# Performance work log

Hardware: AMD Instinct MI355X
Metric: run time of the kernel (lower is better)

The kernel has to match this reference:

```python
import jax, jax.numpy as jnp
import numpy as np
from jax import lax

B, S, D, E, H = 2, 2048, 1024, 8, 4096


def setup_inputs() -> dict:
    key = jax.random.key(0)
    ks = jax.random.split(key, 10)
    sc = 0.02  # GPT-style init scale
    return {
        "x": jax.random.normal(ks[0], (B, S, D), jnp.float32),
        "noise": jax.random.normal(ks[1], (B, S, E), jnp.float32),
        "w_route": jax.random.normal(ks[2], (D, E), jnp.float32) * sc,
        "b_route": jnp.zeros((E,), jnp.float32),
        "w_noise": jax.random.normal(ks[3], (D, E), jnp.float32) * sc,
        "b_noise": jnp.zeros((E,), jnp.float32),
        "w_fc": jax.random.normal(ks[4], (E, D, H), jnp.float32) * sc,
        "b_fc": jnp.zeros((E, H), jnp.float32),
        "w_proj": jax.random.normal(ks[5], (E, H, D), jnp.float32) * sc,
        "b_proj": jnp.zeros((E, D), jnp.float32),
        "top_k": 2,
    }


def reference(x, noise, w_route, b_route, w_noise, b_noise, w_fc, b_fc, w_proj, b_proj, top_k):
    # --- NoisyTopkRouter ---
    logits = x @ w_route + b_route                      # [B,S,E]
    noise_logits = x @ w_noise + b_noise                # [B,S,E]
    noisy = logits + noise * jax.nn.softplus(noise_logits)
    gate1 = jax.nn.softmax(noisy, axis=-1)              # dense gate (aux output)

    topk_vals, topk_idx = lax.top_k(noisy, top_k)       # [B,S,K]
    # softmax over sparse logits (-inf elsewhere) == softmax over the top-k values
    gk = jax.nn.softmax(topk_vals, axis=-1)             # [B,S,K]
    # scatter top-k gates back to the dense expert axis; non-selected experts get 0
    gating = (jax.nn.one_hot(topk_idx, E, dtype=x.dtype) * gk[..., None]).sum(-2)  # [B,S,E]

    # --- Experts (dense-over-experts, masked by gating; math identical to
    #     masked gather/scatter since non-selected gates are exactly 0) ---
    h = jnp.einsum('bsd,edh->bseh', x, w_fc) + b_fc     # [B,S,E,H]
    h = jax.nn.gelu(h, approximate=True)                # GELU(tanh)
    y = jnp.einsum('bseh,ehd->bsed', h, w_proj) + b_proj  # [B,S,E,D]
    out = jnp.einsum('bsed,bse->bsd', y, gating)        # weighted combine
    return out, gate1
```

## Files before the change

### kernel.cpp

```cpp
#include <hip/hip_runtime.h>
#include <cstdint>


#define DEV __device__ __forceinline__

typedef __attribute__((ext_vector_type(8))) short short8;
typedef __attribute__((ext_vector_type(4))) float floatx4;

constexpr int D_ = 1024, E_ = 8, H_ = 4096;
constexpr int NTOK = 4096;
constexpr int CAP  = 4096;
constexpr int TOTSLOT = NTOK * 2;

constexpr size_t O_COUNT = 0;
constexpr size_t O_OFFS  = 64;
constexpr size_t O_BTOK  = 128;
constexpr size_t O_BGATE = O_BTOK  + (size_t)E_ * CAP * 4;
constexpr size_t O_PAIR  = O_BGATE + (size_t)E_ * CAP * 4;
constexpr size_t O_XG    = (O_PAIR + (size_t)NTOK * 2 * 4 + 255) & ~(size_t)255;
constexpr size_t O_HBUF  = O_XG   + (size_t)TOTSLOT * D_ * 2;
constexpr size_t O_YBUF  = O_HBUF + (size_t)TOTSLOT * H_ * 2;
constexpr size_t O_WT    = O_YBUF + (size_t)TOTSLOT * D_ * 2;
constexpr size_t WS_NEED = O_WT   + (size_t)E_ * D_ * H_ * 2;

DEV float b2f(unsigned short u) {
    union { unsigned int i; float f; } v; v.i = ((unsigned int)u) << 16; return v.f;
}
DEV unsigned int f2b(float f) {
    union { float f; unsigned int i; } v; v.f = f;
    unsigned int r = v.i + 0x7fffu + ((v.i >> 16) & 1u);
    return (r >> 16) & 0xffffu;
}
DEV float gelu_tanh(float x) {
    float u = 0.7978845608028654f * (x + 0.044715f * x * x * x);
    u = fminf(fmaxf(u, -20.f), 20.f);
    float e = __expf(2.f * u);
    float t = (e - 1.f) / (e + 1.f);
    return 0.5f * x * (1.f + t);
}

typedef __attribute__((address_space(3))) unsigned int lds_u32_t;
typedef const __attribute__((address_space(1))) unsigned int g_u32_t;
DEV void gload16(const unsigned short* g, const unsigned short* l) {
    __builtin_amdgcn_global_load_lds((g_u32_t*)(size_t)g,
                                     (lds_u32_t*)(unsigned int)(size_t)l, 16, 0, 0);
}

__global__ __launch_bounds__(64) void zero_counts(int* counts) {
    if (threadIdx.x < E_) counts[threadIdx.x] = 0;
}

__global__ __launch_bounds__(256) void router_kernel(
    const float* __restrict__ x, const float* __restrict__ noise,
    const float* __restrict__ w_route, const float* __restrict__ b_route,
    const float* __restrict__ w_noise, const float* __restrict__ b_noise,
    float* __restrict__ out,
    int* counts, int* btok, float* bgate, int* pairs)
{
    int wave = threadIdx.x >> 6, lane = threadIdx.x & 63;
    int t = blockIdx.x * 4 + wave;

    double racc[E_], nacc[E_];
#pragma unroll
    for (int e = 0; e < E_; e++) { racc[e] = 0.0; nacc[e] = 0.0; }

#pragma unroll 4
    for (int i = 0; i < D_ / 64; i++) {
        int j = i * 64 + lane;
        float xv = x[(size_t)t * D_ + j];
        const float* wr = w_route + (size_t)j * E_;
        const float* wn = w_noise + (size_t)j * E_;
        float4 a0 = ((const float4*)wr)[0], a1 = ((const float4*)wr)[1];
        float4 c0 = ((const float4*)wn)[0], c1 = ((const float4*)wn)[1];
        const float rv[8] = {a0.x,a0.y,a0.z,a0.w,a1.x,a1.y,a1.z,a1.w};
        const float nv[8] = {c0.x,c0.y,c0.z,c0.w,c1.x,c1.y,c1.z,c1.w};
#pragma unroll
        for (int e = 0; e < E_; e++) {
            racc[e] += (double)(xv * rv[e]);
            nacc[e] += (double)(xv * nv[e]);
        }
    }
#pragma unroll
    for (int off = 32; off > 0; off >>= 1)
#pragma unroll
        for (int e = 0; e < E_; e++) {
            racc[e] += __shfl_down(racc[e], off);
            nacc[e] += __shfl_down(nacc[e], off);
        }

    if (lane == 0) {
        double nz[E_];
#pragma unroll
        for (int e = 0; e < E_; e++) {
            double lg = racc[e] + (double)b_route[e];
            double nl = nacc[e] + (double)b_noise[e];
            double sp = (nl > 0.0) ? nl + log1p(exp(-nl)) : log1p(exp(nl));
            nz[e] = lg + (double)noise[(size_t)t * E_ + e] * sp;
        }
        double mx = nz[0];
#pragma unroll
        for (int e = 1; e < E_; e++) mx = fmax(mx, nz[e]);
        double se = 0.0, ex[E_];
#pragma unroll
        for (int e = 0; e < E_; e++) { ex[e] = exp(nz[e] - mx); se += ex[e]; }
#pragma unroll
        for (int e = 0; e < E_; e++)
            out[(size_t)NTOK * D_ + (size_t)t * E_ + e] = (float)(ex[e] / se);
        double v0 = -1e300, v1 = -1e300; int i0 = 0, i1 = 0;
#pragma unroll
        for (int e = 0; e < E_; e++) {
            double v = nz[e];
            if (v > v0) { v1 = v0; i1 = i0; v0 = v; i0 = e; }
            else if (v > v1) { v1 = v; i1 = e; }
        }
        double g0 = 1.0 / (1.0 + exp(v1 - v0));
        float  g1 = (float)(1.0 - g0);
        int l0 = atomicAdd(&counts[i0], 1);
        int l1 = atomicAdd(&counts[i1], 1);
        btok[i0 * CAP + l0] = t;  bgate[i0 * CAP + l0] = (float)g0;
        btok[i1 * CAP + l1] = t;  bgate[i1 * CAP + l1] = g1;
        pairs[2 * t]     = (i0 << 16) | l0;
        pairs[2 * t + 1] = (i1 << 16) | l1;
    }
}

__global__ __launch_bounds__(64) void offsets_kernel(const int* counts, int* offs) {
    if (threadIdx.x == 0) {
        int a = 0;
        for (int e = 0; e < E_; e++) { offs[e] = a; a += counts[e]; }
        offs[E_] = a;
    }
}

__global__ __launch_bounds__(256) void gather_x(
    const float* __restrict__ x, const int* __restrict__ pairs,
    const int* __restrict__ offs, unsigned short* __restrict__ xg)
{
    int t = blockIdx.x;
    int c = threadIdx.x * 4;
    float4 v = *(const float4*)(x + (size_t)t * D_ + c);
    uint2 o;
    o.x = f2b(v.x) | (f2b(v.y) << 16);
    o.y = f2b(v.z) | (f2b(v.w) << 16);
    int p0 = pairs[2 * t], p1 = pairs[2 * t + 1];
    size_t r0 = (size_t)(offs[p0 >> 16] + (p0 & 0xffff)) * D_;
    size_t r1 = (size_t)(offs[p1 >> 16] + (p1 & 0xffff)) * D_;
    *(uint2*)(xg + r0 + c) = o;
    *(uint2*)(xg + r1 + c) = o;
}

__global__ __launch_bounds__(256) void transpose_w(
    const float* __restrict__ w, unsigned short* __restrict__ wT, int K, int N)
{
    __shared__ unsigned short t[64][65];
    const int e  = blockIdx.z;
    const int k0 = blockIdx.y * 64;
    const int n0 = blockIdx.x * 64;
    const int r  = threadIdx.x >> 2;
    const int c4 = (threadIdx.x & 3) * 16;
    const float* src = w + ((size_t)e * K + k0 + r) * N + n0 + c4;
#pragma unroll
    for (int i = 0; i < 4; i++) {
        float4 v = ((const float4*)src)[i];
        t[r][c4 + 4*i + 0] = (unsigned short)f2b(v.x);
        t[r][c4 + 4*i + 1] = (unsigned short)f2b(v.y);
        t[r][c4 + 4*i + 2] = (unsigned short)f2b(v.z);
        t[r][c4 + 4*i + 3] = (unsigned short)f2b(v.w);
    }
    __syncthreads();
    unsigned short* dstp = wT + ((size_t)e * N + n0 + r) * K + k0 + c4;
    unsigned short tmp[16];
#pragma unroll
    for (int i = 0; i < 16; i++) tmp[i] = t[c4 + i][r];
#pragma unroll
    for (int h = 0; h < 2; h++) {
        uint4 pk;
        pk.x = (unsigned int)tmp[8*h+0] | ((unsigned int)tmp[8*h+1] << 16);
        pk.y = (unsigned int)tmp[8*h+2] | ((unsigned int)tmp[8*h+3] << 16);
        pk.z = (unsigned int)tmp[8*h+4] | ((unsigned int)tmp[8*h+5] << 16);
        pk.w = (unsigned int)tmp[8*h+6] | ((unsigned int)tmp[8*h+7] << 16);
        ((uint4*)dstp)[h] = pk;
    }
}

template <int KD, int ND, bool FC>
__global__ __launch_bounds__(256) void moe_gemm3(
    const unsigned short* __restrict__ A,
    const unsigned short* __restrict__ wT,
    const float* __restrict__ bias32,
    unsigned short* __restrict__ dst,
    const int* __restrict__ counts, const int* __restrict__ offs,
    const float* __restrict__ bgate)
{
    const int lin = blockIdx.x;
    const int xcd = lin & 7, slot = lin >> 3;
    int e, mt, nt;
    if (FC) {
        nt = xcd * 4 + (slot & 3);
        mt = (slot >> 2) & 31;
        e  = slot >> 7;
    } else {
        nt = xcd;
        mt = slot & 31;
        e  = slot >> 5;
    }
    const int cnt = counts[e];
    const int m0 = mt * 128;
    if (m0 >= cnt) return;
    const int n0 = nt * 128;
    const int off = offs[e];

    __shared__ unsigned short smem[2][2 * 128 * 64];
    constexpr int BOFF = 128 * 64;

    const int tid = threadIdx.x;
    const int waveid = tid >> 6, lane = tid & 63;
    const int sr = lane >> 3;
    const int g  = lane & 7;
    const int scol = ((g ^ sr) * 8);

    const unsigned short* aAddr[4];
    const unsigned short* bAddr[4];
#pragma unroll
    for (int c = 0; c < 4; c++) {
        int ar = m0 + (waveid * 4 + c) * 8 + sr;
        if (ar > cnt - 1) ar = cnt - 1;
        aAddr[c] = A + (size_t)(off + ar) * KD + scol;
        int br = n0 + (waveid * 4 + c) * 8 + sr;
        bAddr[c] = wT + ((size_t)e * ND + br) * KD + scol;
    }
    const int ldsChunk = (waveid * 4) * 512;

    const int wm = (waveid & 1) * 64, wn = (waveid >> 1) * 64;
    const int lrow = lane & 15, quad = lane >> 4;

    floatx4 acc[4][4];
#pragma unroll
    for (int fm = 0; fm < 4; fm++)
#pragma unroll
        for (int fn = 0; fn < 4; fn++) acc[fm][fn] = (floatx4)0.f;

    const int nk = KD / 64;

#pragma unroll
    for (int c = 0; c < 4; c++) {
        gload16(aAddr[c], &smem[0][ldsChunk + c * 512]);
        gload16(bAddr[c], &smem[0][BOFF + ldsChunk + c * 512]);
    }
    __syncthreads();

#pragma unroll 2
    for (int t = 0; t < nk; ++t) {
        const int cur = t & 1;
        if (t + 1 < nk) {
            const int k0 = (t + 1) * 64;
#pragma unroll
            for (int c = 0; c < 4; c++) {
                gload16(aAddr[c] + k0, &smem[cur ^ 1][ldsChunk + c * 512]);
                gload16(bAddr[c] + k0, &smem[cur ^ 1][BOFF + ldsChunk + c * 512]);
            }
        }
        const unsigned short* As = &smem[cur][0];
        const unsigned short* Bs = &smem[cur][BOFF];
#pragma unroll
        for (int ks = 0; ks < 2; ks++) {
            short8 af[4], bfr[4];
#pragma unroll
            for (int f = 0; f < 4; f++) {
                int Ra = wm + f * 16 + lrow;
                int Rb = wn + f * 16 + lrow;
                af[f]  = *(const short8*)&As[Ra * 64 + ((ks * 4 + quad) ^ (Ra & 7)) * 8];
                bfr[f] = *(const short8*)&Bs[Rb * 64 + ((ks * 4 + quad) ^ (Rb & 7)) * 8];
            }
#pragma unroll
            for (int fm = 0; fm < 4; fm++)
#pragma unroll
                for (int fn = 0; fn < 4; fn++)
                    acc[fm][fn] = __builtin_amdgcn_mfma_f32_16x16x32_bf16(
                        af[fm], bfr[fn], acc[fm][fn], 0, 0, 0);
        }
        __syncthreads();
    }

    const int gc = n0 + wn + lrow;
    float bcol[4];
#pragma unroll
    for (int fn = 0; fn < 4; fn++) bcol[fn] = bias32[(size_t)e * ND + gc + fn * 16];

#pragma unroll
    for (int fm = 0; fm < 4; fm++) {
        int srow0 = m0 + wm + fm * 16 + quad * 4;
#pragma unroll
        for (int r = 0; r < 4; r++) {
            int srow = srow0 + r;
            if (srow < cnt) {
                size_t base = (size_t)(off + srow) * ND;
                if (FC) {
#pragma unroll
                    for (int fn = 0; fn < 4; fn++) {
                        float v = acc[fm][fn][r] + bcol[fn];
                        dst[base + gc + fn * 16] = (unsigned short)f2b(gelu_tanh(v));
                    }
                } else {
                    float gt = bgate[e * CAP + srow];
#pragma unroll
                    for (int fn = 0; fn < 4; fn++) {
                        float v = (acc[fm][fn][r] + bcol[fn]) * gt;
                        dst[base + gc + fn * 16] = (unsigned short)f2b(v);
                    }
                }
            }
        }
    }
}

__global__ __launch_bounds__(256) void combine_kernel(
    const unsigned short* __restrict__ ybuf, const int* __restrict__ pairs,
    const int* __restrict__ offs, float* __restrict__ out)
{
    int t = blockIdx.x;
    int p0 = pairs[2 * t], p1 = pairs[2 * t + 1];
    size_t r0 = (size_t)(offs[p0 >> 16] + (p0 & 0xffff)) * D_;
    size_t r1 = (size_t)(offs[p1 >> 16] + (p1 & 0xffff)) * D_;
    int c = threadIdx.x * 4;
    uint2 a = *(const uint2*)(ybuf + r0 + c);
    uint2 b = *(const uint2*)(ybuf + r1 + c);
    float4 o;
    o.x = b2f((unsigned short)(a.x & 0xffffu)) + b2f((unsigned short)(b.x & 0xffffu));
    o.y = b2f((unsigned short)(a.x >> 16))     + b2f((unsigned short)(b.x >> 16));
    o.z = b2f((unsigned short)(a.y & 0xffffu)) + b2f((unsigned short)(b.y & 0xffffu));
    o.w = b2f((unsigned short)(a.y >> 16))     + b2f((unsigned short)(b.y >> 16));
    *(float4*)(out + (size_t)t * D_ + c) = o;
}

extern "C" void kernel_launch(void* const* d_in, const int* in_sizes, int n_in,
                              void* d_out, int out_size, void* d_ws, size_t ws_size,
                              hipStream_t stream) {
    if (ws_size < WS_NEED) return;

    const float* x       = (const float*)d_in[0];
    const float* noise   = (const float*)d_in[1];
    const float* w_route = (const float*)d_in[2];
    const float* b_route = (const float*)d_in[3];
    const float* w_noise = (const float*)d_in[4];
    const float* b_noise = (const float*)d_in[5];
    const float* w_fc    = (const float*)d_in[6];
    const float* b_fc    = (const float*)d_in[7];
    const float* w_proj  = (const float*)d_in[8];
    const float* b_proj  = (const float*)d_in[9];

    char* ws = (char*)d_ws;
    int*   counts = (int*)(ws + O_COUNT);
    int*   offs   = (int*)(ws + O_OFFS);
    int*   btok   = (int*)(ws + O_BTOK);
    float* bgate  = (float*)(ws + O_BGATE);
    int*   pairs  = (int*)(ws + O_PAIR);
    unsigned short* xg   = (unsigned short*)(ws + O_XG);
    unsigned short* hbuf = (unsigned short*)(ws + O_HBUF);
    unsigned short* ybuf = (unsigned short*)(ws + O_YBUF);
    unsigned short* wT   = (unsigned short*)(ws + O_WT);

    zero_counts<<<dim3(1), dim3(64), 0, stream>>>(counts);
    router_kernel<<<dim3(NTOK / 4), dim3(256), 0, stream>>>(
        x, noise, w_route, b_route, w_noise, b_noise, (float*)d_out,
        counts, btok, bgate, pairs);
    offsets_kernel<<<dim3(1), dim3(64), 0, stream>>>(counts, offs);
    gather_x<<<dim3(NTOK), dim3(256), 0, stream>>>(x, pairs, offs, xg);

    transpose_w<<<dim3(H_ / 64, D_ / 64, E_), dim3(256), 0, stream>>>(w_fc, wT, D_, H_);
    moe_gemm3<D_, H_, true><<<dim3(8 * 32 * 32), dim3(256), 0, stream>>>(
        xg, wT, b_fc, hbuf, counts, offs, bgate);

    transpose_w<<<dim3(D_ / 64, H_ / 64, E_), dim3(256), 0, stream>>>(w_proj, wT, H_, D_);
    moe_gemm3<H_, D_, false><<<dim3(8 * 32 * 8), dim3(256), 0, stream>>>(
        hbuf, wT, b_proj, ybuf, counts, offs, bgate);

    combine_kernel<<<dim3(NTOK), dim3(256), 0, stream>>>(ybuf, pairs, offs, (float*)d_out);
}
```

Before: 685.1 us.

## Enlarge MoE GEMM tiles to 256-row blocks with 512 threads

Replaces the 128x128, 256-thread expert GEMM with a templated kernel that uses 256x256 tiles for the FC GEMM and 256x128 tiles for the projection GEMM. It runs 8 waves per block and moves the double buffer into dynamic LDS. The wave-to-tile mapping and the per-wave accumulator count are generalised, and the grid decomposition is recomputed for the larger tiles. The aim is more operand reuse per LDS load and fewer weight re-reads across M tiles. The costs are higher register pressure (up to 128 accumulator registers per lane), a very large LDS footprint (128KB for FC) that limits occupancy to one block per CU, and coarser padding waste on partially filled expert tiles.

```diff
diff --git a/kernel.cpp b/kernel.cpp
--- a/kernel.cpp
+++ b/kernel.cpp
@@ -183,8 +183,8 @@
     }
 }
 
-template <int KD, int ND, bool FC>
-__global__ __launch_bounds__(256) void moe_gemm3(
+template <int BM, int BN, int KD, int ND, bool FC>
+__global__ __launch_bounds__(512, 2) void moe_gemm_big(
     const unsigned short* __restrict__ A,
     const unsigned short* __restrict__ wT,
     const float* __restrict__ bias32,
@@ -192,26 +192,32 @@
     const int* __restrict__ counts, const int* __restrict__ offs,
     const float* __restrict__ bgate)
 {
+    constexpr int SEG  = (BM + BN) * 64;
+    constexpr int BOFF = BM * 64;
+    constexpr int NA   = BM / 64;
+    constexpr int NB   = BN / 64;
+    constexpr int WN   = (BN == 256) ? 4 : 2;
+    constexpr int WTM  = BM / (8 / WN);
+    constexpr int FM   = WTM / 16;
+    extern __shared__ unsigned short smem[];
+
     const int lin = blockIdx.x;
     const int xcd = lin & 7, slot = lin >> 3;
     int e, mt, nt;
     if (FC) {
-        nt = xcd * 4 + (slot & 3);
-        mt = (slot >> 2) & 31;
-        e  = slot >> 7;
+        nt = xcd * 2 + (slot & 1);
+        mt = (slot >> 1) & 15;
+        e  = slot >> 5;
     } else {
         nt = xcd;
-        mt = slot & 31;
-        e  = slot >> 5;
+        mt = slot & 15;
+        e  = slot >> 4;
     }
     const int cnt = counts[e];
-    const int m0 = mt * 128;
+    const int m0 = mt * BM;
     if (m0 >= cnt) return;
-    const int n0 = nt * 128;
+    const int n0 = nt * BN;
     const int off = offs[e];
-
-    __shared__ unsigned short smem[2][2 * 128 * 64];
-    constexpr int BOFF = 128 * 64;
 
     const int tid = threadIdx.x;
     const int waveid = tid >> 6, lane = tid & 63;
@@ -219,34 +225,38 @@
     const int g  = lane & 7;
     const int scol = ((g ^ sr) * 8);
 
-    const unsigned short* aAddr[4];
-    const unsigned short* bAddr[4];
-#pragma unroll
-    for (int c = 0; c < 4; c++) {
-        int ar = m0 + (waveid * 4 + c) * 8 + sr;
+    const unsigned short* aAddr[NA];
+    const unsigned short* bAddr[NB];
+#pragma unroll
+    for (int c = 0; c < NA; c++) {
+        int ar = m0 + (waveid * NA + c) * 8 + sr;
         if (ar > cnt - 1) ar = cnt - 1;
         aAddr[c] = A + (size_t)(off + ar) * KD + scol;
-        int br = n0 + (waveid * 4 + c) * 8 + sr;
+    }
+#pragma unroll
+    for (int c = 0; c < NB; c++) {
+        int br = n0 + (waveid * NB + c) * 8 + sr;
         bAddr[c] = wT + ((size_t)e * ND + br) * KD + scol;
     }
-    const int ldsChunk = (waveid * 4) * 512;
-
-    const int wm = (waveid & 1) * 64, wn = (waveid >> 1) * 64;
+
+    const int wm = (waveid / WN) * WTM;
+    const int wn = (waveid % WN) * 64;
     const int lrow = lane & 15, quad = lane >> 4;
 
-    floatx4 acc[4][4];
-#pragma unroll
-    for (int fm = 0; fm < 4; fm++)
+    floatx4 acc[FM][4];
+#pragma unroll
+    for (int fm = 0; fm < FM; fm++)
 #pragma unroll
         for (int fn = 0; fn < 4; fn++) acc[fm][fn] = (floatx4)0.f;
 
     const int nk = KD / 64;
 
 #pragma unroll
-    for (int c = 0; c < 4; c++) {
-        gload16(aAddr[c], &smem[0][ldsChunk + c * 512]);
-        gload16(bAddr[c], &smem[0][BOFF + ldsChunk + c * 512]);
-    }
+    for (int c = 0; c < NA; c++)
+        gload16(aAddr[c], &smem[(waveid * NA + c) * 512]);
+#pragma unroll
+    for (int c = 0; c < NB; c++)
+        gload16(bAddr[c], &smem[BOFF + (waveid * NB + c) * 512]);
     __syncthreads();
 
 #pragma unroll 2
@@ -254,26 +264,31 @@
         const int cur = t & 1;
         if (t + 1 < nk) {
             const int k0 = (t + 1) * 64;
-#pragma unroll
-            for (int c = 0; c < 4; c++) {
-                gload16(aAddr[c] + k0, &smem[cur ^ 1][ldsChunk + c * 512]);
-                gload16(bAddr[c] + k0, &smem[cur ^ 1][BOFF + ldsChunk + c * 512]);
+            unsigned short* Asn = smem + (cur ^ 1) * SEG;
+#pragma unroll
+            for (int c = 0; c < NA; c++)
+                gload16(aAddr[c] + k0, &Asn[(waveid * NA + c) * 512]);
+#pragma unroll
+            for (int c = 0; c < NB; c++)
+                gload16(bAddr[c] + k0, &Asn[BOFF + (waveid * NB + c) * 512]);
+        }
+        const unsigned short* As = smem + cur * SEG;
+        const unsigned short* Bs = As + BOFF;
+#pragma unroll
+        for (int ks = 0; ks < 2; ks++) {
+            short8 af[FM], bfr[4];
+#pragma unroll
+            for (int f = 0; f < FM; f++) {
+                int Ra = wm + f * 16 + lrow;
+                af[f]  = *(const short8*)&As[Ra * 64 + ((ks * 4 + quad) ^ (Ra & 7)) * 8];
             }
-        }
-        const unsigned short* As = &smem[cur][0];
-        const unsigned short* Bs = &smem[cur][BOFF];
-#pragma unroll
-        for (int ks = 0; ks < 2; ks++) {
-            short8 af[4], bfr[4];
 #pragma unroll
             for (int f = 0; f < 4; f++) {
-                int Ra = wm + f * 16 + lrow;
                 int Rb = wn + f * 16 + lrow;
-                af[f]  = *(const short8*)&As[Ra * 64 + ((ks * 4 + quad) ^ (Ra & 7)) * 8];
                 bfr[f] = *(const short8*)&Bs[Rb * 64 + ((ks * 4 + quad) ^ (Rb & 7)) * 8];
             }
 #pragma unroll
-            for (int fm = 0; fm < 4; fm++)
+            for (int fm = 0; fm < FM; fm++)
 #pragma unroll
                 for (int fn = 0; fn < 4; fn++)
                     acc[fm][fn] = __builtin_amdgcn_mfma_f32_16x16x32_bf16(
@@ -288,7 +303,7 @@
     for (int fn = 0; fn < 4; fn++) bcol[fn] = bias32[(size_t)e * ND + gc + fn * 16];
 
 #pragma unroll
-    for (int fm = 0; fm < 4; fm++) {
+    for (int fm = 0; fm < FM; fm++) {
         int srow0 = m0 + wm + fm * 16 + quad * 4;
 #pragma unroll
         for (int r = 0; r < 4; r++) {
@@ -368,12 +383,20 @@
     gather_x<<<dim3(NTOK), dim3(256), 0, stream>>>(x, pairs, offs, xg);
 
     transpose_w<<<dim3(H_ / 64, D_ / 64, E_), dim3(256), 0, stream>>>(w_fc, wT, D_, H_);
-    moe_gemm3<D_, H_, true><<<dim3(8 * 32 * 32), dim3(256), 0, stream>>>(
-        xg, wT, b_fc, hbuf, counts, offs, bgate);
+    {
+        constexpr unsigned ldsFC = 2u * (256u + 256u) * 64u * 2u;
+        moe_gemm_big<256, 256, D_, H_, true>
+            <<<dim3(8 * 256), dim3(512), ldsFC, stream>>>(
+            xg, wT, b_fc, hbuf, counts, offs, bgate);
+    }
 
     transpose_w<<<dim3(D_ / 64, H_ / 64, E_), dim3(256), 0, stream>>>(w_proj, wT, H_, D_);
-    moe_gemm3<H_, D_, false><<<dim3(8 * 32 * 8), dim3(256), 0, stream>>>(
-        hbuf, wT, b_proj, ybuf, counts, offs, bgate);
+    {
+        constexpr unsigned ldsPJ = 2u * (256u + 128u) * 64u * 2u;
+        moe_gemm_big<256, 128, H_, D_, false>
+            <<<dim3(8 * 128), dim3(512), ldsPJ, stream>>>(
+            hbuf, wT, b_proj, ybuf, counts, offs, bgate);
+    }
 
     combine_kernel<<<dim3(NTOK), dim3(256), 0, stream>>>(ybuf, pairs, offs, (float*)d_out);
 }
```

After: 702.2 us. 2.5% more time.

## Split-K the projection GEMM with fp32 atomics and shrink K-tile to 32

Applied to the files above, without the earlier changes.

The projection GEMM is split into two K halves so it launches twice as many blocks. Each half accumulates its partial results into zeroed fp32 buffers with atomicAdd, and the combine kernel now reads fp32 instead of bf16. Both GEMMs now use a 32-wide K tile with a new LDS swizzle, which halves shared memory and raises the number of loop iterations. This adds a zeroing pass, atomic traffic and twice the fp32 output bandwidth, and it reuses the xg and ybuf workspace regions for the partial buffers.

```diff
diff --git a/kernel.cpp b/kernel.cpp
--- a/kernel.cpp
+++ b/kernel.cpp
@@ -183,26 +183,36 @@
     }
 }
 
-template <int KD, int ND, bool FC>
-__global__ __launch_bounds__(256) void moe_gemm3(
+__global__ __launch_bounds__(256) void zero_pbuf(float* pb0, float* pb1) {
+    size_t i = ((size_t)blockIdx.x * 256 + threadIdx.x) * 4;
+    float4 z = {0.f, 0.f, 0.f, 0.f};
+    *(float4*)(pb0 + i) = z;
+    *(float4*)(pb1 + i) = z;
+}
+
+template <int KD, int ND, bool FC, int KHALVES>
+__global__ __launch_bounds__(256) void moe_gemm32(
     const unsigned short* __restrict__ A,
     const unsigned short* __restrict__ wT,
     const float* __restrict__ bias32,
-    unsigned short* __restrict__ dst,
+    unsigned short* __restrict__ dstBf,
+    float* __restrict__ pb0, float* __restrict__ pb1,
     const int* __restrict__ counts, const int* __restrict__ offs,
     const float* __restrict__ bgate)
 {
     const int lin = blockIdx.x;
     const int xcd = lin & 7, slot = lin >> 3;
-    int e, mt, nt;
+    int e, mt, nt, kh;
     if (FC) {
         nt = xcd * 4 + (slot & 3);
         mt = (slot >> 2) & 31;
         e  = slot >> 7;
+        kh = 0;
     } else {
         nt = xcd;
         mt = slot & 31;
-        e  = slot >> 5;
+        kh = (slot >> 5) & 1;
+        e  = slot >> 6;
     }
     const int cnt = counts[e];
     const int m0 = mt * 128;
@@ -210,26 +220,29 @@
     const int n0 = nt * 128;
     const int off = offs[e];
 
-    __shared__ unsigned short smem[2][2 * 128 * 64];
-    constexpr int BOFF = 128 * 64;
+    constexpr int KB = KD / KHALVES;
+    const int kbase = kh * KB;
+
+    __shared__ unsigned short smem[2][2 * 128 * 32];
+    constexpr int BOFF = 128 * 32;
 
     const int tid = threadIdx.x;
     const int waveid = tid >> 6, lane = tid & 63;
-    const int sr = lane >> 3;
-    const int g  = lane & 7;
-    const int scol = ((g ^ sr) * 8);
-
-    const unsigned short* aAddr[4];
-    const unsigned short* bAddr[4];
-#pragma unroll
-    for (int c = 0; c < 4; c++) {
-        int ar = m0 + (waveid * 4 + c) * 8 + sr;
+    const int srow16 = lane >> 2;
+    const int sslot  = lane & 3;
+
+    const unsigned short* aAddr[2];
+    const unsigned short* bAddr[2];
+#pragma unroll
+    for (int c = 0; c < 2; c++) {
+        const int rl = (waveid * 2 + c) * 16 + srow16;
+        const int g  = sslot ^ ((rl >> 1) & 3);
+        int ar = m0 + rl;
         if (ar > cnt - 1) ar = cnt - 1;
-        aAddr[c] = A + (size_t)(off + ar) * KD + scol;
-        int br = n0 + (waveid * 4 + c) * 8 + sr;
-        bAddr[c] = wT + ((size_t)e * ND + br) * KD + scol;
-    }
-    const int ldsChunk = (waveid * 4) * 512;
+        aAddr[c] = A + (size_t)(off + ar) * KD + kbase + g * 8;
+        const int br = n0 + rl;
+        bAddr[c] = wT + ((size_t)e * ND + br) * KD + kbase + g * 8;
+    }
 
     const int wm = (waveid & 1) * 64, wn = (waveid >> 1) * 64;
     const int lrow = lane & 15, quad = lane >> 4;
@@ -240,45 +253,41 @@
 #pragma unroll
         for (int fn = 0; fn < 4; fn++) acc[fm][fn] = (floatx4)0.f;
 
-    const int nk = KD / 64;
-
-#pragma unroll
-    for (int c = 0; c < 4; c++) {
-        gload16(aAddr[c], &smem[0][ldsChunk + c * 512]);
-        gload16(bAddr[c], &smem[0][BOFF + ldsChunk + c * 512]);
+    const int nk = KB / 32;
+
+#pragma unroll
+    for (int c = 0; c < 2; c++) {
+        gload16(aAddr[c], &smem[0][(waveid * 2 + c) * 512]);
+        gload16(bAddr[c], &smem[0][BOFF + (waveid * 2 + c) * 512]);
     }
     __syncthreads();
 
-#pragma unroll 2
     for (int t = 0; t < nk; ++t) {
         const int cur = t & 1;
         if (t + 1 < nk) {
-            const int k0 = (t + 1) * 64;
-#pragma unroll
-            for (int c = 0; c < 4; c++) {
-                gload16(aAddr[c] + k0, &smem[cur ^ 1][ldsChunk + c * 512]);
-                gload16(bAddr[c] + k0, &smem[cur ^ 1][BOFF + ldsChunk + c * 512]);
+            const int k0 = (t + 1) * 32;
+#pragma unroll
+            for (int c = 0; c < 2; c++) {
+                gload16(aAddr[c] + k0, &smem[cur ^ 1][(waveid * 2 + c) * 512]);
+                gload16(bAddr[c] + k0, &smem[cur ^ 1][BOFF + (waveid * 2 + c) * 512]);
             }
         }
         const unsigned short* As = &smem[cur][0];
         const unsigned short* Bs = &smem[cur][BOFF];
-#pragma unroll
-        for (int ks = 0; ks < 2; ks++) {
-            short8 af[4], bfr[4];
-#pragma unroll
-            for (int f = 0; f < 4; f++) {
-                int Ra = wm + f * 16 + lrow;
-                int Rb = wn + f * 16 + lrow;
-                af[f]  = *(const short8*)&As[Ra * 64 + ((ks * 4 + quad) ^ (Ra & 7)) * 8];
-                bfr[f] = *(const short8*)&Bs[Rb * 64 + ((ks * 4 + quad) ^ (Rb & 7)) * 8];
-            }
-#pragma unroll
-            for (int fm = 0; fm < 4; fm++)
-#pragma unroll
-                for (int fn = 0; fn < 4; fn++)
-                    acc[fm][fn] = __builtin_amdgcn_mfma_f32_16x16x32_bf16(
-                        af[fm], bfr[fn], acc[fm][fn], 0, 0, 0);
-        }
+        short8 af[4], bfr[4];
+#pragma unroll
+        for (int f = 0; f < 4; f++) {
+            const int Ra = wm + f * 16 + lrow;
+            const int Rb = wn + f * 16 + lrow;
+            af[f]  = *(const short8*)&As[Ra * 32 + ((quad ^ ((Ra >> 1) & 3)) * 8)];
+            bfr[f] = *(const short8*)&Bs[Rb * 32 + ((quad ^ ((Rb >> 1) & 3)) * 8)];
+        }
+#pragma unroll
+        for (int fm = 0; fm < 4; fm++)
+#pragma unroll
+            for (int fn = 0; fn < 4; fn++)
+                acc[fm][fn] = __builtin_amdgcn_mfma_f32_16x16x32_bf16(
+                    af[fm], bfr[fn], acc[fm][fn], 0, 0, 0);
         __syncthreads();
     }
 
@@ -294,19 +303,23 @@
         for (int r = 0; r < 4; r++) {
             int srow = srow0 + r;
             if (srow < cnt) {
-                size_t base = (size_t)(off + srow) * ND;
+                const int oslot = off + srow;
                 if (FC) {
+                    size_t base = (size_t)oslot * ND;
 #pragma unroll
                     for (int fn = 0; fn < 4; fn++) {
                         float v = acc[fm][fn][r] + bcol[fn];
-                        dst[base + gc + fn * 16] = (unsigned short)f2b(gelu_tanh(v));
+                        dstBf[base + gc + fn * 16] = (unsigned short)f2b(gelu_tanh(v));
                     }
                 } else {
                     float gt = bgate[e * CAP + srow];
+                    float* pb = (oslot < NTOK)
+                        ? pb0 + (size_t)oslot * ND
+                        : pb1 + (size_t)(oslot - NTOK) * ND;
 #pragma unroll
                     for (int fn = 0; fn < 4; fn++) {
-                        float v = (acc[fm][fn][r] + bcol[fn]) * gt;
-                        dst[base + gc + fn * 16] = (unsigned short)f2b(v);
+                        float v = (acc[fm][fn][r] + (kh == 0 ? bcol[fn] : 0.f)) * gt;
+                        atomicAdd(&pb[gc + fn * 16], v);
                     }
                 }
             }
@@ -315,21 +328,23 @@
 }
 
 __global__ __launch_bounds__(256) void combine_kernel(
-    const unsigned short* __restrict__ ybuf, const int* __restrict__ pairs,
-    const int* __restrict__ offs, float* __restrict__ out)
+    const float* __restrict__ pb0, const float* __restrict__ pb1,
+    const int* __restrict__ pairs, const int* __restrict__ offs,
+    float* __restrict__ out)
 {
     int t = blockIdx.x;
     int p0 = pairs[2 * t], p1 = pairs[2 * t + 1];
-    size_t r0 = (size_t)(offs[p0 >> 16] + (p0 & 0xffff)) * D_;
-    size_t r1 = (size_t)(offs[p1 >> 16] + (p1 & 0xffff)) * D_;
+    int s0 = offs[p0 >> 16] + (p0 & 0xffff);
+    int s1 = offs[p1 >> 16] + (p1 & 0xffff);
     int c = threadIdx.x * 4;
-    uint2 a = *(const uint2*)(ybuf + r0 + c);
-    uint2 b = *(const uint2*)(ybuf + r1 + c);
+    const float* a = (s0 < NTOK ? pb0 + (size_t)s0 * D_
+                                : pb1 + (size_t)(s0 - NTOK) * D_) + c;
+    const float* b = (s1 < NTOK ? pb0 + (size_t)s1 * D_
+                                : pb1 + (size_t)(s1 - NTOK) * D_) + c;
+    float4 va = *(const float4*)a;
+    float4 vb = *(const float4*)b;
     float4 o;
-    o.x = b2f((unsigned short)(a.x & 0xffffu)) + b2f((unsigned short)(b.x & 0xffffu));
-    o.y = b2f((unsigned short)(a.x >> 16))     + b2f((unsigned short)(b.x >> 16));
-    o.z = b2f((unsigned short)(a.y & 0xffffu)) + b2f((unsigned short)(b.y & 0xffffu));
-    o.w = b2f((unsigned short)(a.y >> 16))     + b2f((unsigned short)(b.y >> 16));
+    o.x = va.x + vb.x; o.y = va.y + vb.y; o.z = va.z + vb.z; o.w = va.w + vb.w;
     *(float4*)(out + (size_t)t * D_ + c) = o;
 }
 
@@ -357,8 +372,9 @@
     int*   pairs  = (int*)(ws + O_PAIR);
     unsigned short* xg   = (unsigned short*)(ws + O_XG);
     unsigned short* hbuf = (unsigned short*)(ws + O_HBUF);
-    unsigned short* ybuf = (unsigned short*)(ws + O_YBUF);
     unsigned short* wT   = (unsigned short*)(ws + O_WT);
+    float* pb0 = (float*)(ws + O_XG);
+    float* pb1 = (float*)(ws + O_YBUF);
 
     zero_counts<<<dim3(1), dim3(64), 0, stream>>>(counts);
     router_kernel<<<dim3(NTOK / 4), dim3(256), 0, stream>>>(
@@ -368,12 +384,14 @@
     gather_x<<<dim3(NTOK), dim3(256), 0, stream>>>(x, pairs, offs, xg);
 
     transpose_w<<<dim3(H_ / 64, D_ / 64, E_), dim3(256), 0, stream>>>(w_fc, wT, D_, H_);
-    moe_gemm3<D_, H_, true><<<dim3(8 * 32 * 32), dim3(256), 0, stream>>>(
-        xg, wT, b_fc, hbuf, counts, offs, bgate);
+    moe_gemm32<D_, H_, true, 1><<<dim3(8 * 32 * 32), dim3(256), 0, stream>>>(
+        xg, wT, b_fc, hbuf, pb0, pb1, counts, offs, bgate);
+
+    zero_pbuf<<<dim3(NTOK), dim3(256), 0, stream>>>(pb0, pb1);
 
     transpose_w<<<dim3(D_ / 64, H_ / 64, E_), dim3(256), 0, stream>>>(w_proj, wT, H_, D_);
-    moe_gemm3<H_, D_, false><<<dim3(8 * 32 * 8), dim3(256), 0, stream>>>(
-        hbuf, wT, b_proj, ybuf, counts, offs, bgate);
-
-    combine_kernel<<<dim3(NTOK), dim3(256), 0, stream>>>(ybuf, pairs, offs, (float*)d_out);
-}
+    moe_gemm32<H_, D_, false, 2><<<dim3(8 * 32 * 2 * 8), dim3(256), 0, stream>>>(
+        hbuf, wT, b_proj, nullptr, pb0, pb1, counts, offs, bgate);
+
+    combine_kernel<<<dim3(NTOK), dim3(256), 0, stream>>>(pb0, pb1, pairs, offs, (float*)d_out);
+}
```

After: 704.0 us. +2.8%, slower.
